# Optimization experiments

Measured on AMD Instinct MI355X. Metric: run time of the kernel, lower is better.

Reference implementation:

```python
import jax, jax.numpy as jnp
import numpy as np

N_NODES = 50000
N_EDGES = 800000
N_FEAT = 256


def setup_inputs() -> dict:
    key = jax.random.key(0)
    k_h, k_src, k_dst, k_w1, k_w2 = jax.random.split(key, 5)
    h = jax.random.normal(k_h, (N_NODES, N_FEAT), dtype=jnp.float32)
    src = jax.random.randint(k_src, (N_EDGES,), 0, N_NODES, dtype=jnp.int32)
    dst = jax.random.randint(k_dst, (N_EDGES,), 0, N_NODES, dtype=jnp.int32)
    # Kaiming-uniform-ish init like nn.Linear defaults
    b1 = 1.0 / np.sqrt(2 * N_FEAT)
    b2 = 1.0 / np.sqrt(N_FEAT)
    W1_w = jax.random.uniform(k_w1, (N_FEAT, 2 * N_FEAT), dtype=jnp.float32, minval=-b1, maxval=b1)
    W1_b = jnp.zeros((N_FEAT,), dtype=jnp.float32)
    W2_w = jax.random.uniform(k_w2, (1, N_FEAT), dtype=jnp.float32, minval=-b2, maxval=b2)
    W2_b = jnp.zeros((1,), dtype=jnp.float32)
    return {"h": h, "src": src, "dst": dst, "W1_w": W1_w, "W1_b": W1_b, "W2_w": W2_w, "W2_b": W2_b}


def reference(h, src, dst, W1_w, W1_b, W2_w, W2_b):
    # Gather per-edge endpoint features and concat along feature dim: [E, 2F]
    e = jnp.concatenate([h[src], h[dst]], axis=-1)
    # 2-layer MLP: Linear -> ReLU -> Linear, squeeze to per-edge score [E]
    hid = jax.nn.relu(e @ W1_w.T + W1_b)          # [E, F]
    score = (hid @ W2_w.T + W2_b)[:, 0]            # [E]
    return score
```

## Files before the change

kernel.cpp:

```cpp
#include <hip/hip_runtime.h>

#define F 256
#define TWO_F 512
#define BM 128
#define BN 64
#define BK 64

typedef __attribute__((ext_vector_type(8))) short short8;
typedef __attribute__((ext_vector_type(4))) float float4v;

static __device__ __forceinline__ unsigned short f2bf(float f) {
    unsigned u = __float_as_uint(f);
    u += 0x7FFFu + ((u >> 16) & 1u);
    return (unsigned short)(u >> 16);
}
static __device__ __forceinline__ unsigned pack2(float lo, float hi) {
    unsigned a = __float_as_uint(lo) + 0x8000u;
    unsigned b = __float_as_uint(hi) + 0x8000u;
    return __builtin_amdgcn_perm(b, a, 0x07060302u);
}
static __device__ __forceinline__ float blo(unsigned u) { return __uint_as_float(u << 16); }
static __device__ __forceinline__ float rawf(unsigned u) { return __uint_as_float(u); }

__global__ __launch_bounds__(256) void prep_kernel(
    const float* __restrict__ h, const float* __restrict__ W1,
    unsigned short* __restrict__ hb, unsigned short* __restrict__ Wb, int M)
{
    int i = blockIdx.x * blockDim.x + threadIdx.x;
    if (i < M * 128) {
        int m = i >> 7;
        int kp = (i & 127) * 2;
        float2 v = *(const float2*)(h + (size_t)m * F + kp);
        unsigned pk = pack2(v.x, v.y);
        int ksw = ((kp & 63) + (m & 7) * 8) & 63;
        *(unsigned*)(hb + (size_t)m * F + (kp & ~63) + ksw) = pk;
    }
    if (i < TWO_F * F) {
        int n = i >> 8;
        int k = i & 255;
        float v = W1[(n & 255) * TWO_F + ((n >> 8) << 8) + k];
        int kin_sw = ((k & 63) + (n & 7) * 8) & 63;
        Wb[n * F + (k & ~63) + kin_sw] = f2bf(v);
    }
}

__global__ __launch_bounds__(256, 4) void gemm_kernel(
    const unsigned short* __restrict__ hb, const unsigned short* __restrict__ Wb,
    const float* __restrict__ b1v, unsigned short* __restrict__ C, int M)
{
    __shared__ unsigned short sA[BM * BK];
    __shared__ unsigned short sB[BN * BK];

    const int ib = blockIdx.x;
    const int r8 = ib & 7;
    const int q  = ib >> 3;
    const int by = q & 7;
    const int bx = (q >> 3) * 8 + r8;
    const int bm = bx * BM;
    if (bm >= M) return;
    const int bn = by * BN;

    const int tid  = threadIdx.x;
    const int lane = tid & 63;
    const int wid  = tid >> 6;
    const int st_r = lane >> 3;
    const int st_k = (lane & 7) * 8;
    const int quad = lane >> 4;
    const int l15  = lane & 15;
    const int rot  = (l15 & 7) * 8;

    float4v acc[2][4];
    #pragma unroll
    for (int i = 0; i < 2; ++i)
        #pragma unroll
        for (int j = 0; j < 4; ++j) acc[i][j] = (float4v)(0.f);

    for (int k0 = 0; k0 < F; k0 += BK) {
        #pragma unroll
        for (int p = 0; p < 4; ++p) {
            int r = wid * 32 + p * 8;
            int am = bm + r + st_r; if (am > M - 1) am = M - 1;
            const unsigned short* ga = hb + (size_t)am * F + k0 + st_k;
            __builtin_amdgcn_global_load_lds(
                (const __attribute__((address_space(1))) unsigned int*)ga,
                (__attribute__((address_space(3))) unsigned int*)&sA[r * BK],
                16, 0, 0);
        }
        #pragma unroll
        for (int p = 0; p < 2; ++p) {
            int r = wid * 16 + p * 8;
            const unsigned short* gb = Wb + (size_t)(bn + r + st_r) * F + k0 + st_k;
            __builtin_amdgcn_global_load_lds(
                (const __attribute__((address_space(1))) unsigned int*)gb,
                (__attribute__((address_space(3))) unsigned int*)&sB[r * BK],
                16, 0, 0);
        }
        __syncthreads();

        #pragma unroll
        for (int ks = 0; ks < 2; ++ks) {
            const int koff = (ks * 32 + quad * 8 + rot) & 63;
            short8 afr[2], bfr[4];
            #pragma unroll
            for (int mt = 0; mt < 2; ++mt)
                afr[mt] = *(const short8*)&sA[(wid * 32 + mt * 16 + l15) * BK + koff];
            #pragma unroll
            for (int nt = 0; nt < 4; ++nt)
                bfr[nt] = *(const short8*)&sB[(nt * 16 + l15) * BK + koff];
            #pragma unroll
            for (int mt = 0; mt < 2; ++mt)
                #pragma unroll
                for (int nt = 0; nt < 4; ++nt)
                    acc[mt][nt] = __builtin_amdgcn_mfma_f32_16x16x32_bf16(
                        afr[mt], bfr[nt], acc[mt][nt], 0, 0, 0);
        }
        __syncthreads();
    }

    float bias[4];
    #pragma unroll
    for (int nt = 0; nt < 4; ++nt) {
        int n = bn + nt * 16 + l15;
        bias[nt] = (n < F) ? b1v[n] : 0.f;
    }
    #pragma unroll
    for (int mt = 0; mt < 2; ++mt) {
        #pragma unroll
        for (int rr = 0; rr < 4; ++rr) {
            int row = wid * 32 + mt * 16 + quad * 4 + rr;
            #pragma unroll
            for (int nt = 0; nt < 4; ++nt)
                sA[row * BK + nt * 16 + l15] = f2bf(acc[mt][nt][rr] + bias[nt]);
        }
    }
    __syncthreads();
    #pragma unroll
    for (int p = 0; p < 4; ++p) {
        int row = p * 32 + (tid >> 3);
        int gm = bm + row;
        if (gm < M) {
            uint4 v = *(const uint4*)&sA[row * BK + (tid & 7) * 8];
            *(uint4*)(C + (size_t)gm * TWO_F + bn + (tid & 7) * 8) = v;
        }
    }
}

__global__ __launch_bounds__(256) void edge_kernel(
    const unsigned short* __restrict__ C,
    const int* __restrict__ src, const int* __restrict__ dst,
    const float* __restrict__ w2,
    const float* __restrict__ b2, float* __restrict__ out, int E)
{
    const int lane = threadIdx.x & 31;
    const int g = blockIdx.x * 8 + (threadIdx.x >> 5);
    const int e0 = g * 2;
    if (e0 >= E) return;
    const int s0 = src[e0], d0 = dst[e0];
    const int s1 = src[e0 + 1], d1 = dst[e0 + 1];

    uint4 av0 = *(const uint4*)(C + (size_t)s0 * TWO_F + lane * 8);
    uint4 bv0 = *(const uint4*)(C + (size_t)d0 * TWO_F + F + lane * 8);
    uint4 av1 = *(const uint4*)(C + (size_t)s1 * TWO_F + lane * 8);
    uint4 bv1 = *(const uint4*)(C + (size_t)d1 * TWO_F + F + lane * 8);
    float4 w0 = *(const float4*)(w2 + lane * 8);
    float4 w1 = *(const float4*)(w2 + lane * 8 + 4);

    float sum0, sum1;
    sum0  = w0.x * fmaxf(blo(av0.x) + blo(bv0.x), 0.f);
    sum0 += w0.y * fmaxf(rawf(av0.x) + rawf(bv0.x), 0.f);
    sum0 += w0.z * fmaxf(blo(av0.y) + blo(bv0.y), 0.f);
    sum0 += w0.w * fmaxf(rawf(av0.y) + rawf(bv0.y), 0.f);
    sum0 += w1.x * fmaxf(blo(av0.z) + blo(bv0.z), 0.f);
    sum0 += w1.y * fmaxf(rawf(av0.z) + rawf(bv0.z), 0.f);
    sum0 += w1.z * fmaxf(blo(av0.w) + blo(bv0.w), 0.f);
    sum0 += w1.w * fmaxf(rawf(av0.w) + rawf(bv0.w), 0.f);

    sum1  = w0.x * fmaxf(blo(av1.x) + blo(bv1.x), 0.f);
    sum1 += w0.y * fmaxf(rawf(av1.x) + rawf(bv1.x), 0.f);
    sum1 += w0.z * fmaxf(blo(av1.y) + blo(bv1.y), 0.f);
    sum1 += w0.w * fmaxf(rawf(av1.y) + rawf(bv1.y), 0.f);
    sum1 += w1.x * fmaxf(blo(av1.z) + blo(bv1.z), 0.f);
    sum1 += w1.y * fmaxf(rawf(av1.z) + rawf(bv1.z), 0.f);
    sum1 += w1.z * fmaxf(blo(av1.w) + blo(bv1.w), 0.f);
    sum1 += w1.w * fmaxf(rawf(av1.w) + rawf(bv1.w), 0.f);

    #pragma unroll
    for (int off = 16; off > 0; off >>= 1) {
        sum0 += __shfl_down(sum0, off, 32);
        sum1 += __shfl_down(sum1, off, 32);
    }

    if (lane == 0) {
        float b = b2[0];
        out[e0]     = sum0 + b;
        out[e0 + 1] = sum1 + b;
    }
}

extern "C" void kernel_launch(void* const* d_in, const int* in_sizes, int n_in,
                              void* d_out, int out_size, void* d_ws, size_t ws_size,
                              hipStream_t stream) {
    const float* h    = (const float*)d_in[0];
    const int*   src  = (const int*)d_in[1];
    const int*   dst  = (const int*)d_in[2];
    const float* W1_w = (const float*)d_in[3];
    const float* W1_b = (const float*)d_in[4];
    const float* W2_w = (const float*)d_in[5];
    const float* W2_b = (const float*)d_in[6];
    float* out = (float*)d_out;

    const int M = in_sizes[0] / F;
    const int E = in_sizes[1];

    unsigned short* Wb = (unsigned short*)d_ws;
    unsigned short* hb = (unsigned short*)((char*)d_ws + 512 * 1024);
    unsigned short* C  = (unsigned short*)((char*)d_ws + 512 * 1024 + 26 * 1024 * 1024);

    int prep_threads = M * 128 > TWO_F * F ? M * 128 : TWO_F * F;
    prep_kernel<<<(prep_threads + 255) / 256, 256, 0, stream>>>(h, W1_w, hb, Wb, M);

    int nbx = ((M + BM - 1) / BM + 7) / 8 * 8;
    gemm_kernel<<<nbx * 8, 256, 0, stream>>>(hb, Wb, W1_b, C, M);

    edge_kernel<<<(E / 2 + 7) / 8, 256, 0, stream>>>(C, src, dst, W2_w, W2_b, out, E);
}
```

Baseline: 225.3 us.

## Fuse bf16 conversion into GEMM and bucket-sort edges by source for gather locality

Removes the separate prep kernel. The GEMM now converts W1 to swizzled bf16 in LDS and reads fp32 rows of h straight from global memory, packing them into MFMA fragments in registers. This avoids writing and rereading a bf16 copy of h. A new kernel buckets edges by src>>7 into fixed-size padded buckets with atomics, and the edge kernel walks those buckets so source-row gathers from C are more local. The fixed bucket capacity (PAD) and bucket count assume a roughly uniform edge distribution and this node count. The sort adds extra passes and atomics, and the scatter writes to out become irregular.

```diff
diff --git a/kernel.cpp b/kernel.cpp
--- a/kernel.cpp
+++ b/kernel.cpp
@@ -4,7 +4,9 @@
 #define TWO_F 512
 #define BM 128
 #define BN 64
-#define BK 64
+#define NBUCK 391
+#define PAD 2560
+#define EPB 8192
 
 typedef __attribute__((ext_vector_type(8))) short short8;
 typedef __attribute__((ext_vector_type(4))) float float4v;
@@ -22,34 +24,11 @@
 static __device__ __forceinline__ float blo(unsigned u) { return __uint_as_float(u << 16); }
 static __device__ __forceinline__ float rawf(unsigned u) { return __uint_as_float(u); }
 
-__global__ __launch_bounds__(256) void prep_kernel(
+__global__ __launch_bounds__(256, 4) void gemm_kernel(
     const float* __restrict__ h, const float* __restrict__ W1,
-    unsigned short* __restrict__ hb, unsigned short* __restrict__ Wb, int M)
-{
-    int i = blockIdx.x * blockDim.x + threadIdx.x;
-    if (i < M * 128) {
-        int m = i >> 7;
-        int kp = (i & 127) * 2;
-        float2 v = *(const float2*)(h + (size_t)m * F + kp);
-        unsigned pk = pack2(v.x, v.y);
-        int ksw = ((kp & 63) + (m & 7) * 8) & 63;
-        *(unsigned*)(hb + (size_t)m * F + (kp & ~63) + ksw) = pk;
-    }
-    if (i < TWO_F * F) {
-        int n = i >> 8;
-        int k = i & 255;
-        float v = W1[(n & 255) * TWO_F + ((n >> 8) << 8) + k];
-        int kin_sw = ((k & 63) + (n & 7) * 8) & 63;
-        Wb[n * F + (k & ~63) + kin_sw] = f2bf(v);
-    }
-}
-
-__global__ __launch_bounds__(256, 4) void gemm_kernel(
-    const unsigned short* __restrict__ hb, const unsigned short* __restrict__ Wb,
     const float* __restrict__ b1v, unsigned short* __restrict__ C, int M)
 {
-    __shared__ unsigned short sA[BM * BK];
-    __shared__ unsigned short sB[BN * BK];
+    __shared__ unsigned short sB[BN * F];
 
     const int ib = blockIdx.x;
     const int r8 = ib & 7;
@@ -63,50 +42,61 @@
     const int tid  = threadIdx.x;
     const int lane = tid & 63;
     const int wid  = tid >> 6;
-    const int st_r = lane >> 3;
-    const int st_k = (lane & 7) * 8;
     const int quad = lane >> 4;
     const int l15  = lane & 15;
     const int rot  = (l15 & 7) * 8;
 
+    {
+        int nn = tid >> 2;
+        int kb = (tid & 3) * 64;
+        int n  = bn + nn;
+        const float* wrow = W1 + (size_t)(n & 255) * TWO_F + ((n >> 8) << 8) + kb;
+        #pragma unroll
+        for (int c = 0; c < 8; ++c) {
+            float4 va = *(const float4*)(wrow + c * 8);
+            float4 vb = *(const float4*)(wrow + c * 8 + 4);
+            unsigned u0 = pack2(va.x, va.y), u1 = pack2(va.z, va.w);
+            unsigned u2 = pack2(vb.x, vb.y), u3 = pack2(vb.z, vb.w);
+            int p0 = (c * 8 + (nn & 7) * 8) & 63;
+            unsigned* dsp = (unsigned*)&sB[nn * F + kb + p0];
+            dsp[0] = u0; dsp[1] = u1; dsp[2] = u2; dsp[3] = u3;
+        }
+    }
+
+    const float* arow[2];
+    #pragma unroll
+    for (int mt = 0; mt < 2; ++mt) {
+        int am = bm + wid * 32 + mt * 16 + l15;
+        if (am > M - 1) am = M - 1;
+        arow[mt] = h + (size_t)am * F;
+    }
+
     float4v acc[2][4];
     #pragma unroll
     for (int i = 0; i < 2; ++i)
         #pragma unroll
         for (int j = 0; j < 4; ++j) acc[i][j] = (float4v)(0.f);
 
-    for (int k0 = 0; k0 < F; k0 += BK) {
-        #pragma unroll
-        for (int p = 0; p < 4; ++p) {
-            int r = wid * 32 + p * 8;
-            int am = bm + r + st_r; if (am > M - 1) am = M - 1;
-            const unsigned short* ga = hb + (size_t)am * F + k0 + st_k;
-            __builtin_amdgcn_global_load_lds(
-                (const __attribute__((address_space(1))) unsigned int*)ga,
-                (__attribute__((address_space(3))) unsigned int*)&sA[r * BK],
-                16, 0, 0);
-        }
-        #pragma unroll
-        for (int p = 0; p < 2; ++p) {
-            int r = wid * 16 + p * 8;
-            const unsigned short* gb = Wb + (size_t)(bn + r + st_r) * F + k0 + st_k;
-            __builtin_amdgcn_global_load_lds(
-                (const __attribute__((address_space(1))) unsigned int*)gb,
-                (__attribute__((address_space(3))) unsigned int*)&sB[r * BK],
-                16, 0, 0);
-        }
-        __syncthreads();
-
+    __syncthreads();
+
+    #pragma unroll
+    for (int kt = 0; kt < 4; ++kt) {
         #pragma unroll
         for (int ks = 0; ks < 2; ++ks) {
-            const int koff = (ks * 32 + quad * 8 + rot) & 63;
+            const int ka  = kt * 64 + ks * 32 + quad * 8;
+            const int kbo = kt * 64 + ((ks * 32 + quad * 8 + rot) & 63);
             short8 afr[2], bfr[4];
             #pragma unroll
-            for (int mt = 0; mt < 2; ++mt)
-                afr[mt] = *(const short8*)&sA[(wid * 32 + mt * 16 + l15) * BK + koff];
+            for (int mt = 0; mt < 2; ++mt) {
+                float4 fa = *(const float4*)(arow[mt] + ka);
+                float4 fb = *(const float4*)(arow[mt] + ka + 4);
+                unsigned* ap = (unsigned*)&afr[mt];
+                ap[0] = pack2(fa.x, fa.y); ap[1] = pack2(fa.z, fa.w);
+                ap[2] = pack2(fb.x, fb.y); ap[3] = pack2(fb.z, fb.w);
+            }
             #pragma unroll
             for (int nt = 0; nt < 4; ++nt)
-                bfr[nt] = *(const short8*)&sB[(nt * 16 + l15) * BK + koff];
+                bfr[nt] = *(const short8*)&sB[(nt * 16 + l15) * F + kbo];
             #pragma unroll
             for (int mt = 0; mt < 2; ++mt)
                 #pragma unroll
@@ -114,7 +104,6 @@
                     acc[mt][nt] = __builtin_amdgcn_mfma_f32_16x16x32_bf16(
                         afr[mt], bfr[nt], acc[mt][nt], 0, 0, 0);
         }
-        __syncthreads();
     }
 
     float bias[4];
@@ -123,6 +112,7 @@
         int n = bn + nt * 16 + l15;
         bias[nt] = (n < F) ? b1v[n] : 0.f;
     }
+    __syncthreads();
     #pragma unroll
     for (int mt = 0; mt < 2; ++mt) {
         #pragma unroll
@@ -130,7 +120,7 @@
             int row = wid * 32 + mt * 16 + quad * 4 + rr;
             #pragma unroll
             for (int nt = 0; nt < 4; ++nt)
-                sA[row * BK + nt * 16 + l15] = f2bf(acc[mt][nt][rr] + bias[nt]);
+                sB[row * BN + nt * 16 + l15] = f2bf(acc[mt][nt][rr] + bias[nt]);
         }
     }
     __syncthreads();
@@ -139,29 +129,78 @@
         int row = p * 32 + (tid >> 3);
         int gm = bm + row;
         if (gm < M) {
-            uint4 v = *(const uint4*)&sA[row * BK + (tid & 7) * 8];
+            uint4 v = *(const uint4*)&sB[row * BN + (tid & 7) * 8];
             *(uint4*)(C + (size_t)gm * TWO_F + bn + (tid & 7) * 8) = v;
+        }
+    }
+}
+
+__global__ __launch_bounds__(256) void sort_scatter_kernel(
+    const int* __restrict__ src, const int* __restrict__ dst,
+    int* __restrict__ cursor, int2* __restrict__ sort_sd,
+    int* __restrict__ sort_idx, int E)
+{
+    __shared__ int hist[512];
+    __shared__ int base[512];
+    const int tid = threadIdx.x;
+    #pragma unroll
+    for (int i = tid; i < 512; i += 256) hist[i] = 0;
+    __syncthreads();
+    const int bs = blockIdx.x * EPB;
+    #pragma unroll
+    for (int j = 0; j < EPB / 256; ++j) {
+        int e = bs + j * 256 + tid;
+        if (e < E) atomicAdd(&hist[((unsigned)src[e]) >> 7], 1);
+    }
+    __syncthreads();
+    #pragma unroll
+    for (int i = tid; i < 512; i += 256) {
+        int c = hist[i];
+        base[i] = c ? atomicAdd(&cursor[i], c) : 0;
+        hist[i] = 0;
+    }
+    __syncthreads();
+    #pragma unroll
+    for (int j = 0; j < EPB / 256; ++j) {
+        int e = bs + j * 256 + tid;
+        if (e < E) {
+            int s = src[e];
+            int bkt = ((unsigned)s) >> 7;
+            int r = atomicAdd(&hist[bkt], 1);
+            int pos = bkt * PAD + base[bkt] + r;
+            sort_sd[pos] = make_int2(s, dst[e]);
+            sort_idx[pos] = e;
         }
     }
 }
 
 __global__ __launch_bounds__(256) void edge_kernel(
     const unsigned short* __restrict__ C,
-    const int* __restrict__ src, const int* __restrict__ dst,
+    const int2* __restrict__ sd, const int* __restrict__ sidx,
+    const int* __restrict__ fill,
     const float* __restrict__ w2,
-    const float* __restrict__ b2, float* __restrict__ out, int E)
+    const float* __restrict__ b2, float* __restrict__ out)
 {
     const int lane = threadIdx.x & 31;
-    const int g = blockIdx.x * 8 + (threadIdx.x >> 5);
-    const int e0 = g * 2;
-    if (e0 >= E) return;
-    const int s0 = src[e0], d0 = dst[e0];
-    const int s1 = src[e0 + 1], d1 = dst[e0 + 1];
-
-    uint4 av0 = *(const uint4*)(C + (size_t)s0 * TWO_F + lane * 8);
-    uint4 bv0 = *(const uint4*)(C + (size_t)d0 * TWO_F + F + lane * 8);
-    uint4 av1 = *(const uint4*)(C + (size_t)s1 * TWO_F + lane * 8);
-    uint4 bv1 = *(const uint4*)(C + (size_t)d1 * TWO_F + F + lane * 8);
+    const int nblk = gridDim.x;
+    const int ib = blockIdx.x;
+    const int gb = (ib & 7) * (nblk >> 3) + (ib >> 3);
+    const int g = gb * 8 + (threadIdx.x >> 5);
+    const int sl0 = g * 2;
+    const int bkt = sl0 / PAD;
+    const int o = sl0 - bkt * PAD;
+    const int cnt = fill[bkt];
+    if (o >= cnt) return;
+    const bool has1 = (o + 1 < cnt);
+    int2 p0 = sd[sl0];
+    int2 p1 = has1 ? sd[sl0 + 1] : p0;
+    int i0 = sidx[sl0];
+    int i1 = has1 ? sidx[sl0 + 1] : 0;
+
+    uint4 av0 = *(const uint4*)(C + (size_t)p0.x * TWO_F + lane * 8);
+    uint4 bv0 = *(const uint4*)(C + (size_t)p0.y * TWO_F + F + lane * 8);
+    uint4 av1 = *(const uint4*)(C + (size_t)p1.x * TWO_F + lane * 8);
+    uint4 bv1 = *(const uint4*)(C + (size_t)p1.y * TWO_F + F + lane * 8);
     float4 w0 = *(const float4*)(w2 + lane * 8);
     float4 w1 = *(const float4*)(w2 + lane * 8 + 4);
 
@@ -192,8 +231,8 @@
 
     if (lane == 0) {
         float b = b2[0];
-        out[e0]     = sum0 + b;
-        out[e0 + 1] = sum1 + b;
+        out[i0] = sum0 + b;
+        if (has1) out[i1] = sum1 + b;
     }
 }
 
@@ -212,15 +251,19 @@
     const int M = in_sizes[0] / F;
     const int E = in_sizes[1];
 
-    unsigned short* Wb = (unsigned short*)d_ws;
-    unsigned short* hb = (unsigned short*)((char*)d_ws + 512 * 1024);
-    unsigned short* C  = (unsigned short*)((char*)d_ws + 512 * 1024 + 26 * 1024 * 1024);
-
-    int prep_threads = M * 128 > TWO_F * F ? M * 128 : TWO_F * F;
-    prep_kernel<<<(prep_threads + 255) / 256, 256, 0, stream>>>(h, W1_w, hb, Wb, M);
+    int2* sort_sd  = (int2*)d_ws;
+    int*  sort_idx = (int*)((char*)d_ws + 9 * 1024 * 1024);
+    int*  cursor   = (int*)((char*)d_ws + 14 * 1024 * 1024);
+    unsigned short* C = (unsigned short*)((char*)d_ws + 512 * 1024 + 26 * 1024 * 1024);
+
+    hipMemsetAsync(cursor, 0, 512 * sizeof(int), stream);
 
     int nbx = ((M + BM - 1) / BM + 7) / 8 * 8;
-    gemm_kernel<<<nbx * 8, 256, 0, stream>>>(hb, Wb, W1_b, C, M);
-
-    edge_kernel<<<(E / 2 + 7) / 8, 256, 0, stream>>>(C, src, dst, W2_w, W2_b, out, E);
-}
+    gemm_kernel<<<nbx * 8, 256, 0, stream>>>(h, W1_w, W1_b, C, M);
+
+    sort_scatter_kernel<<<(E + EPB - 1) / EPB, 256, 0, stream>>>(
+        src, dst, cursor, sort_sd, sort_idx, E);
+
+    edge_kernel<<<NBUCK * PAD / 16, 256, 0, stream>>>(
+        C, sort_sd, sort_idx, cursor, W2_w, W2_b, out);
+}
```

New measurement: 273.1 us. 21.2% more time.

## Double-buffer LDS tiles in GEMM with explicit waitcnt pipeline

Applied to the files above, without the earlier changes.

The GEMM k-loop now uses two LDS buffers for the A and B tiles, is fully unrolled over the four k-steps, and prefetches the next tile while computing on the current one. It uses manual s_waitcnt vmcnt and barriers instead of a __syncthreads pair per step. The goal is to hide global-to-LDS load latency behind MFMA work. In exchange, LDS use doubles and the occupancy hint drops from 4 to 3 blocks per CU.

```diff
diff --git a/kernel.cpp b/kernel.cpp
--- a/kernel.cpp
+++ b/kernel.cpp
@@ -44,12 +44,12 @@
     }
 }
 
-__global__ __launch_bounds__(256, 4) void gemm_kernel(
+__global__ __launch_bounds__(256, 3) void gemm_kernel(
     const unsigned short* __restrict__ hb, const unsigned short* __restrict__ Wb,
     const float* __restrict__ b1v, unsigned short* __restrict__ C, int M)
 {
-    __shared__ unsigned short sA[BM * BK];
-    __shared__ unsigned short sB[BN * BK];
+    __shared__ unsigned short sA[2][BM * BK];
+    __shared__ unsigned short sB[2][BN * BK];
 
     const int ib = blockIdx.x;
     const int r8 = ib & 7;
@@ -75,7 +75,7 @@
         #pragma unroll
         for (int j = 0; j < 4; ++j) acc[i][j] = (float4v)(0.f);
 
-    for (int k0 = 0; k0 < F; k0 += BK) {
+    auto stage = [&](int buf, int k0) {
         #pragma unroll
         for (int p = 0; p < 4; ++p) {
             int r = wid * 32 + p * 8;
@@ -83,7 +83,7 @@
             const unsigned short* ga = hb + (size_t)am * F + k0 + st_k;
             __builtin_amdgcn_global_load_lds(
                 (const __attribute__((address_space(1))) unsigned int*)ga,
-                (__attribute__((address_space(3))) unsigned int*)&sA[r * BK],
+                (__attribute__((address_space(3))) unsigned int*)&sA[buf][r * BK],
                 16, 0, 0);
         }
         #pragma unroll
@@ -92,21 +92,22 @@
             const unsigned short* gb = Wb + (size_t)(bn + r + st_r) * F + k0 + st_k;
             __builtin_amdgcn_global_load_lds(
                 (const __attribute__((address_space(1))) unsigned int*)gb,
-                (__attribute__((address_space(3))) unsigned int*)&sB[r * BK],
+                (__attribute__((address_space(3))) unsigned int*)&sB[buf][r * BK],
                 16, 0, 0);
         }
-        __syncthreads();
-
+    };
+
+    auto compute = [&](int cur) {
         #pragma unroll
         for (int ks = 0; ks < 2; ++ks) {
             const int koff = (ks * 32 + quad * 8 + rot) & 63;
             short8 afr[2], bfr[4];
             #pragma unroll
             for (int mt = 0; mt < 2; ++mt)
-                afr[mt] = *(const short8*)&sA[(wid * 32 + mt * 16 + l15) * BK + koff];
+                afr[mt] = *(const short8*)&sA[cur][(wid * 32 + mt * 16 + l15) * BK + koff];
             #pragma unroll
             for (int nt = 0; nt < 4; ++nt)
-                bfr[nt] = *(const short8*)&sB[(nt * 16 + l15) * BK + koff];
+                bfr[nt] = *(const short8*)&sB[cur][(nt * 16 + l15) * BK + koff];
             #pragma unroll
             for (int mt = 0; mt < 2; ++mt)
                 #pragma unroll
@@ -114,8 +115,7 @@
                     acc[mt][nt] = __builtin_amdgcn_mfma_f32_16x16x32_bf16(
                         afr[mt], bfr[nt], acc[mt][nt], 0, 0, 0);
         }
-        __syncthreads();
-    }
+    };
 
     float bias[4];
     #pragma unroll
@@ -123,6 +123,40 @@
         int n = bn + nt * 16 + l15;
         bias[nt] = (n < F) ? b1v[n] : 0.f;
     }
+    __builtin_amdgcn_sched_barrier(0);
+
+    stage(0, 0);
+    __builtin_amdgcn_sched_barrier(0);
+    stage(1, 64);
+    __builtin_amdgcn_sched_barrier(0);
+    asm volatile("s_waitcnt vmcnt(6)" ::: "memory");
+    __builtin_amdgcn_s_barrier();
+
+    compute(0);
+    asm volatile("s_waitcnt lgkmcnt(0)" ::: "memory");
+    __builtin_amdgcn_sched_barrier(0);
+    __builtin_amdgcn_s_barrier();
+    stage(0, 128);
+    __builtin_amdgcn_sched_barrier(0);
+    asm volatile("s_waitcnt vmcnt(6)" ::: "memory");
+    __builtin_amdgcn_s_barrier();
+
+    compute(1);
+    asm volatile("s_waitcnt lgkmcnt(0)" ::: "memory");
+    __builtin_amdgcn_sched_barrier(0);
+    __builtin_amdgcn_s_barrier();
+    stage(1, 192);
+    __builtin_amdgcn_sched_barrier(0);
+    asm volatile("s_waitcnt vmcnt(6)" ::: "memory");
+    __builtin_amdgcn_s_barrier();
+
+    compute(0);
+    asm volatile("s_waitcnt vmcnt(0)" ::: "memory");
+    __builtin_amdgcn_s_barrier();
+
+    compute(1);
+
+    __syncthreads();
     #pragma unroll
     for (int mt = 0; mt < 2; ++mt) {
         #pragma unroll
@@ -130,7 +164,7 @@
             int row = wid * 32 + mt * 16 + quad * 4 + rr;
             #pragma unroll
             for (int nt = 0; nt < 4; ++nt)
-                sA[row * BK + nt * 16 + l15] = f2bf(acc[mt][nt][rr] + bias[nt]);
+                sA[0][row * BK + nt * 16 + l15] = f2bf(acc[mt][nt][rr] + bias[nt]);
         }
     }
     __syncthreads();
@@ -139,7 +173,7 @@
         int row = p * 32 + (tid >> 3);
         int gm = bm + row;
         if (gm < M) {
-            uint4 v = *(const uint4*)&sA[row * BK + (tid & 7) * 8];
+            uint4 v = *(const uint4*)&sA[0][row * BK + (tid & 7) * 8];
             *(uint4*)(C + (size_t)gm * TWO_F + bn + (tid & 7) * 8) = v;
         }
     }
```

Result: no change. 227.0 us (+0.8%).
